# Optimization experiments

Hardware: AMD Instinct MI355X
Metric: run time of the kernel (lower is better)

## Reference

```python
import jax, jax.numpy as jnp
import numpy as np

LR = 0.01            # learning_rate
PC = 0.001           # pred_clipping
WC = 5.0             # weight_clipping
_LO = float(np.log(PC / (1.0 - PC)))   # logit(pred_clipping)
_HI = -_LO                              # logit(1 - pred_clipping)


def setup_inputs() -> dict:
    B, S, I, CTX, M, C = 64, 1023, 1024, 784, 4, 1  # S = size-1 (bias row), C = num_classes->1
    key = jax.random.key(0)
    k = jax.random.split(key, 6)
    logit = jax.random.normal(k[0], (B, I, C), jnp.float32)
    context = jax.random.normal(k[1], (B, CTX), jnp.float32)
    target = jax.random.uniform(k[2], (B, C), dtype=jnp.float32)
    cm = jax.random.normal(k[3], (C, S, M, CTX), jnp.float32)
    cm = cm / jnp.linalg.norm(cm, axis=-1, keepdims=True)          # unit-norm context maps
    cb = jax.random.normal(k[4], (C, S, M, 1), jnp.float32)        # context bias
    weights = jnp.full((C, S, 2 ** M, I), 1.0 / I, jnp.float32)    # per-context weight table
    bias = jax.random.uniform(k[5], (1, 1, C), jnp.float32, _LO, _HI)
    return {"logit": logit, "context": context, "target": target,
            "context_maps": cm, "context_bias": cb, "weights": weights, "bias": bias}


def reference(logit, context, target, context_maps, context_bias, weights, bias):
    C, S, M, _ = context_maps.shape
    B = context.shape[0]
    # halfspace hashing of the context -> per-(class, neuron, sample) weight-table index
    dist = jnp.einsum('csmk,bk->csmb', context_maps, context)      # [C,S,M,B]
    bits = (dist > context_bias).astype(jnp.int32)
    conv = (2 ** jnp.arange(M, dtype=jnp.int32))[:, None]          # [M,1]
    idx = jnp.sum(bits * conv, axis=-2)                            # [C,S,B] in [0, 2^M)
    ci = jnp.arange(C)[:, None, None]
    si = jnp.arange(S)[None, :, None]
    sel = weights[ci, si, idx]                                     # gather -> [C,S,B,I]
    # batched dot product (torch code does full matmul + diagonal; this is the same math)
    out = jnp.clip(jnp.einsum('csbi,bic->csb', sel, logit), _LO, _HI)
    out_bsc = out.transpose(2, 1, 0)                               # [B,S,C]
    # online weight update (target branch): gather-compute-scatter
    diff = jax.nn.sigmoid(out_bsc) - target[:, None, :]            # [B,S,C]
    upd = LR * diff[..., None] * logit.transpose(0, 2, 1)[:, None, :, :]  # [B,S,C,I]
    new_sel = jnp.clip(sel - upd.transpose(2, 1, 0, 3), -WC, WC)   # [C,S,B,I]
    new_weights = weights.at[ci, si, idx].set(new_sel)             # scatter
    # prepend constant bias neuron
    out_logits = jnp.concatenate([jnp.broadcast_to(bias, (B, 1, C)), out_bsc], axis=1)  # [B,S+1,C]
    return out_logits, new_weights
```

## Files before the change

kernel.cpp:

```cpp
#include <hip/hip_runtime.h>
#include <math.h>

typedef unsigned long long u64;
typedef __attribute__((ext_vector_type(8))) short bf16x8;
typedef __attribute__((ext_vector_type(4))) float f32x4;

#define S_DIM 1023
#define B_DIM 64
#define I_DIM 1024
#define CTX_DIM 784
#define CTX4 196
#define NWROWS 16

#define LR_C 0.01f
#define WC_C 5.0f
#define LO_C (-6.906754778648554f)
#define HI_C ( 6.906754778648554f)

__device__ __forceinline__ float dot4(float4 a, float4 b) {
    return a.x * b.x + a.y * b.y + a.z * b.z + a.w * b.w;
}

__device__ __forceinline__ float4 upd4(float4 w, float4 a, float c) {
    float4 r;
    r.x = fminf(fmaxf(w.x - c * a.x, -WC_C), WC_C);
    r.y = fminf(fmaxf(w.y - c * a.y, -WC_C), WC_C);
    r.z = fminf(fmaxf(w.z - c * a.z, -WC_C), WC_C);
    r.w = fminf(fmaxf(w.w - c * a.w, -WC_C), WC_C);
    return r;
}

__device__ __forceinline__ short f2bf(float f) {
    union { float f; unsigned u; } cv; cv.f = f;
    unsigned r = cv.u + 0x7fffu + ((cv.u >> 16) & 1u);
    return (short)(r >> 16);
}

__device__ __forceinline__ float bf2f(short h) {
    union { unsigned u; float f; } cv;
    cv.u = ((unsigned)(unsigned short)h) << 16;
    return cv.f;
}

__global__ __launch_bounds__(256) void prep_pack_kernel(
    const float* __restrict__ context,
    const float* __restrict__ bias,
    const float* __restrict__ logit,
    float4* __restrict__ ctxT4,
    short* __restrict__ pack_b,
    float* __restrict__ out_logits)
{
    const int blk = blockIdx.x;
    const int t = threadIdx.x;
    if (blk < 49) {
        int g = blk * 256 + t;
        int k4 = g >> 6;
        int b  = g & 63;
        ctxT4[g] = *(const float4*)(context + (size_t)b * CTX_DIM + k4 * 4);
        if (g < B_DIM) out_logits[(size_t)g * (S_DIM + 1)] = bias[0];
    } else {
        int g = (blk - 49) * 256 + t;
        int l  = g & 63;
        int kb = (g >> 6) & 31;
        int nt = g >> 11;
        int b  = nt * 16 + (l & 15);
        int i0 = kb * 32 + (l >> 4) * 8;
        const float* src = logit + (size_t)b * I_DIM + i0;
        bf16x8 v;
        #pragma unroll
        for (int j = 0; j < 8; ++j) v[j] = f2bf(src[j]);
        *(bf16x8*)(pack_b + (size_t)g * 8) = v;
    }
}

__global__ __launch_bounds__(256) void gln_idx_kernel(
    const float* __restrict__ cm,
    const float* __restrict__ cb,
    const float4* __restrict__ ctxT4,
    u64* __restrict__ mask_g)
{
    __shared__ float red[4][4][64];
    __shared__ int   bits[4][64];
    __shared__ float cb_lds[4];

    const int s = blockIdx.x;
    const int t = threadIdx.x;
    if (t < 4) cb_lds[t] = cb[s * 4 + t];

    const int b = t & 63;
    const int q = __builtin_amdgcn_readfirstlane(t >> 6);
    const float4* cmr = (const float4*)(cm + (size_t)s * 4 * CTX_DIM);

    float a0 = 0.f, a1 = 0.f, a2 = 0.f, a3 = 0.f;
    const int k0 = q * 49;
    #pragma unroll 7
    for (int kk = 0; kk < 49; ++kk) {
        int k4 = k0 + kk;
        float4 c4 = ctxT4[k4 * 64 + b];
        a0 += dot4(cmr[k4], c4);
        a1 += dot4(cmr[CTX4 + k4], c4);
        a2 += dot4(cmr[2 * CTX4 + k4], c4);
        a3 += dot4(cmr[3 * CTX4 + k4], c4);
    }
    red[q][0][b] = a0;
    red[q][1][b] = a1;
    red[q][2][b] = a2;
    red[q][3][b] = a3;
    __syncthreads();

    {
        int m = t >> 6, bb = t & 63;
        float sum = red[0][m][bb] + red[1][m][bb] + red[2][m][bb] + red[3][m][bb];
        bits[m][bb] = (sum > cb_lds[m]) ? 1 : 0;
    }
    __syncthreads();

    if (t < B_DIM) {
        int v = bits[0][t] + 2 * bits[1][t] + 4 * bits[2][t] + 8 * bits[3][t];
        u64 my = 0;
        #pragma unroll
        for (int kk = 0; kk < NWROWS; ++kk) {
            u64 mk = __ballot(v == kk);
            if (t == kk) my = mk;
        }
        if (t < NWROWS) mask_g[s * NWROWS + t] = my;
    }
}

__global__ __launch_bounds__(256, 4) void gln_body_kernel(
    const float* __restrict__ logit,
    const float* __restrict__ target,
    const float* __restrict__ weights,
    const u64*   __restrict__ mask_g,
    const short* __restrict__ pack_b,
    float* __restrict__ out_logits,
    float* __restrict__ new_weights)
{
    __shared__ short Abf[NWROWS * I_DIM];
    __shared__ u64   mask_lds[NWROWS];
    __shared__ int   lastb_lds[NWROWS];
    __shared__ float coef_lds[NWROWS];

    const int s  = blockIdx.x;
    const int t  = threadIdx.x;
    const int wv = t >> 6;
    const int l  = t & 63;

    if (t < NWROWS) {
        u64 m = mask_g[s * NWROWS + t];
        mask_lds[t]  = m;
        lastb_lds[t] = m ? (63 - __clzll(m)) : -1;
    }

    const float4* W4 = (const float4*)(weights + (size_t)s * (NWROWS * I_DIM));
    #pragma unroll
    for (int j = 0; j < 16; ++j) {
        float4 w = W4[t + j * 256];
        int slot = j * 128 + ((t >> 1) ^ (j & 7));
        short4 v;
        v.x = f2bf(w.x); v.y = f2bf(w.y); v.z = f2bf(w.z); v.w = f2bf(w.w);
        *(short4*)(Abf + slot * 8 + (t & 1) * 4) = v;
    }
    __syncthreads();

    const int row = l & 15;
    const int q2  = l >> 4;
    const int sw  = row & 7;
    const int base_slot = row * 128;
    const bf16x8* Bb = (const bf16x8*)pack_b + (size_t)wv * 2048 + l;
    f32x4 acc = {0.f, 0.f, 0.f, 0.f};
    #pragma unroll 8
    for (int kb = 0; kb < 32; ++kb) {
        bf16x8 af = *(const bf16x8*)(Abf + 8 * (base_slot + ((kb * 4 + q2) ^ sw)));
        bf16x8 bfr = Bb[(size_t)kb * 64];
        acc = __builtin_amdgcn_mfma_f32_16x16x32_bf16(af, bfr, acc, 0, 0, 0);
    }

    const int col = wv * 16 + (l & 15);
    #pragma unroll
    for (int j = 0; j < 4; ++j) {
        int r = q2 * 4 + j;
        u64 m = mask_lds[r];
        if ((m >> col) & 1) {
            float o = fminf(fmaxf(acc[j], LO_C), HI_C);
            out_logits[(size_t)col * (S_DIM + 1) + s + 1] = o;
            if (col == lastb_lds[r])
                coef_lds[r] = LR_C * (1.0f / (1.0f + expf(-o)) - target[col]);
        }
    }
    __syncthreads();

    float4*       D4 = (float4*)(new_weights + (size_t)s * (NWROWS * I_DIM));
    const float4* L4 = (const float4*)logit;
    #pragma unroll 4
    for (int r = 0; r < NWROWS; ++r) {
        const int lb = lastb_lds[r];
        int slot = r * 128 + ((t >> 1) ^ (r & 7));
        short4 v = *(const short4*)(Abf + slot * 8 + (t & 1) * 4);
        float4 w;
        w.x = bf2f(v.x); w.y = bf2f(v.y); w.z = bf2f(v.z); w.w = bf2f(v.w);
        float4 o;
        if (lb < 0) {
            o = w;
        } else {
            o = upd4(w, L4[lb * 256 + t], coef_lds[r]);
        }
        D4[r * 256 + t] = o;
    }
}

extern "C" void kernel_launch(void* const* d_in, const int* in_sizes, int n_in,
                              void* d_out, int out_size, void* d_ws, size_t ws_size,
                              hipStream_t stream) {
    const float* logit   = (const float*)d_in[0];
    const float* context = (const float*)d_in[1];
    const float* target  = (const float*)d_in[2];
    const float* cm      = (const float*)d_in[3];
    const float* cb      = (const float*)d_in[4];
    const float* weights = (const float*)d_in[5];
    const float* bias    = (const float*)d_in[6];

    float* out_logits  = (float*)d_out;
    float* new_weights = out_logits + (size_t)B_DIM * (S_DIM + 1);

    char* ws = (char*)d_ws;
    float4* ctxT4  = (float4*)ws;    ws += (size_t)CTX4 * B_DIM * 16;
    short*  packb  = (short*)ws;     ws += (size_t)4 * 32 * 64 * 8 * 2;
    u64*    mask_g = (u64*)ws;

    prep_pack_kernel<<<81, 256, 0, stream>>>(context, bias, logit, ctxT4, packb, out_logits);
    gln_idx_kernel<<<S_DIM, 256, 0, stream>>>(cm, cb, ctxT4, mask_g);
    gln_body_kernel<<<S_DIM, 256, 0, stream>>>(logit, target, weights, mask_g, packb,
                                               out_logits, new_weights);
}
```

Baseline: 52.71 us.

## Split each neuron's weight table across two blocks of eight rows

Measured after the change: 53.47 us. No clear change (+1.4%).

```diff
diff --git a/kernel.cpp b/kernel.cpp
--- a/kernel.cpp
+++ b/kernel.cpp
@@ -11,6 +11,7 @@
 #define CTX_DIM 784
 #define CTX4 196
 #define NWROWS 16
+#define HROWS 8
 
 #define LR_C 0.01f
 #define WC_C 5.0f
@@ -127,7 +128,7 @@
     }
 }
 
-__global__ __launch_bounds__(256, 4) void gln_body_kernel(
+__global__ __launch_bounds__(256, 8) void gln_body_kernel(
     const float* __restrict__ logit,
     const float* __restrict__ target,
     const float* __restrict__ weights,
@@ -136,66 +137,71 @@
     float* __restrict__ out_logits,
     float* __restrict__ new_weights)
 {
-    __shared__ short Abf[NWROWS * I_DIM];
-    __shared__ u64   mask_lds[NWROWS];
-    __shared__ int   lastb_lds[NWROWS];
-    __shared__ float coef_lds[NWROWS];
-
-    const int s  = blockIdx.x;
+    __shared__ short Abf[HROWS * I_DIM];
+    __shared__ u64   mask_lds[HROWS];
+    __shared__ int   lastb_lds[HROWS];
+    __shared__ float coef_lds[HROWS];
+
+    const int blk  = blockIdx.x;
+    const int s    = blk >> 1;
+    const int half = blk & 1;
     const int t  = threadIdx.x;
     const int wv = t >> 6;
     const int l  = t & 63;
 
-    if (t < NWROWS) {
-        u64 m = mask_g[s * NWROWS + t];
+    if (t < HROWS) {
+        u64 m = mask_g[s * NWROWS + half * HROWS + t];
         mask_lds[t]  = m;
         lastb_lds[t] = m ? (63 - __clzll(m)) : -1;
     }
 
-    const float4* W4 = (const float4*)(weights + (size_t)s * (NWROWS * I_DIM));
+    const float4* W4 = (const float4*)(weights
+                     + (size_t)s * (NWROWS * I_DIM) + (size_t)half * (HROWS * I_DIM));
     #pragma unroll
-    for (int j = 0; j < 16; ++j) {
+    for (int j = 0; j < HROWS; ++j) {
         float4 w = W4[t + j * 256];
-        int slot = j * 128 + ((t >> 1) ^ (j & 7));
+        int slot = j * 128 + ((t >> 1) ^ j);
         short4 v;
         v.x = f2bf(w.x); v.y = f2bf(w.y); v.z = f2bf(w.z); v.w = f2bf(w.w);
         *(short4*)(Abf + slot * 8 + (t & 1) * 4) = v;
     }
     __syncthreads();
 
-    const int row = l & 15;
+    const int row_local = l & 7;
     const int q2  = l >> 4;
-    const int sw  = row & 7;
-    const int base_slot = row * 128;
+    const int base_slot = row_local * 128;
     const bf16x8* Bb = (const bf16x8*)pack_b + (size_t)wv * 2048 + l;
     f32x4 acc = {0.f, 0.f, 0.f, 0.f};
     #pragma unroll 8
     for (int kb = 0; kb < 32; ++kb) {
-        bf16x8 af = *(const bf16x8*)(Abf + 8 * (base_slot + ((kb * 4 + q2) ^ sw)));
+        bf16x8 af = *(const bf16x8*)(Abf + 8 * (base_slot + ((kb * 4 + q2) ^ row_local)));
         bf16x8 bfr = Bb[(size_t)kb * 64];
         acc = __builtin_amdgcn_mfma_f32_16x16x32_bf16(af, bfr, acc, 0, 0, 0);
     }
 
     const int col = wv * 16 + (l & 15);
-    #pragma unroll
-    for (int j = 0; j < 4; ++j) {
-        int r = q2 * 4 + j;
-        u64 m = mask_lds[r];
-        if ((m >> col) & 1) {
-            float o = fminf(fmaxf(acc[j], LO_C), HI_C);
-            out_logits[(size_t)col * (S_DIM + 1) + s + 1] = o;
-            if (col == lastb_lds[r])
-                coef_lds[r] = LR_C * (1.0f / (1.0f + expf(-o)) - target[col]);
+    if (q2 < 2) {
+        #pragma unroll
+        for (int j = 0; j < 4; ++j) {
+            int r = q2 * 4 + j;
+            u64 m = mask_lds[r];
+            if ((m >> col) & 1) {
+                float o = fminf(fmaxf(acc[j], LO_C), HI_C);
+                out_logits[(size_t)col * (S_DIM + 1) + s + 1] = o;
+                if (col == lastb_lds[r])
+                    coef_lds[r] = LR_C * (1.0f / (1.0f + expf(-o)) - target[col]);
+            }
         }
     }
     __syncthreads();
 
-    float4*       D4 = (float4*)(new_weights + (size_t)s * (NWROWS * I_DIM));
+    float4* D4 = (float4*)(new_weights
+               + (size_t)s * (NWROWS * I_DIM) + (size_t)half * (HROWS * I_DIM));
     const float4* L4 = (const float4*)logit;
     #pragma unroll 4
-    for (int r = 0; r < NWROWS; ++r) {
+    for (int r = 0; r < HROWS; ++r) {
         const int lb = lastb_lds[r];
-        int slot = r * 128 + ((t >> 1) ^ (r & 7));
+        int slot = r * 128 + ((t >> 1) ^ r);
         short4 v = *(const short4*)(Abf + slot * 8 + (t & 1) * 4);
         float4 w;
         w.x = bf2f(v.x); w.y = bf2f(v.y); w.z = bf2f(v.z); w.w = bf2f(v.w);
@@ -230,6 +236,6 @@
 
     prep_pack_kernel<<<81, 256, 0, stream>>>(context, bias, logit, ctxT4, packb, out_logits);
     gln_idx_kernel<<<S_DIM, 256, 0, stream>>>(cm, cb, ctxT4, mask_g);
-    gln_body_kernel<<<S_DIM, 256, 0, stream>>>(logit, target, weights, mask_g, packb,
-                                               out_logits, new_weights);
-}
+    gln_body_kernel<<<S_DIM * 2, 256, 0, stream>>>(logit, target, weights, mask_g, packb,
+                                                   out_logits, new_weights);
+}
```
